# Optimization experiments

Measured on AMD Instinct MI355X. Metric: run time of the kernel, lower is better.

The kernel has to match this reference:

```python
import math
import jax, jax.numpy as jnp
import numpy as np

B, S, DK, DV = 8, 2048, 512, 512

def setup_inputs() -> dict:
    key = jax.random.key(0)
    kq, kk, kv, km = jax.random.split(key, 4)
    Q = jax.random.normal(kq, (B, S, DK), dtype=jnp.float32)
    K = jax.random.normal(kk, (B, S, DK), dtype=jnp.float32)
    V = jax.random.normal(kv, (B, S, DV), dtype=jnp.float32)
    # key-padding mask, True = masked out; broadcasts over query dim
    mask_out = jax.random.randint(km, (B, 1, S), 0, 2).astype(jnp.bool_)
    return {"Q": Q, "K": K, "V": V, "mask_out": mask_out}

def reference(Q, K, V, mask_out):
    scale = math.sqrt(Q.shape[-1])
    # [B, S, S] scores
    scores = jnp.einsum('bqd,bkd->bqk', Q, K) / scale
    scores = jnp.where(mask_out, -jnp.inf, scores)
    attn = jax.nn.softmax(scores, axis=-1)
    # dropout is identity in eval mode (reference baseline)
    return jnp.einsum('bqk,bkv->bqv', attn, V)
```

## Files before the change

kernel.cpp:

```cpp
#include <hip/hip_runtime.h>
#include <stdint.h>
#include <stddef.h>

#define B_ 8
#define S_ 2048
#define D_ 512
#define QT 64
#define KTL 32
#define NIT (S_ / KTL)

typedef __attribute__((ext_vector_type(8))) short short8;
typedef __attribute__((ext_vector_type(4))) float f32x4;

#define OFF_K0  0
#define OFF_K1  32768
#define OFF_ST  65536
#define OFF_P   73728
#define OFF_A   77824
#define OFF_L   78080
#define OFF_M   78336
#define LDS_BYTES 78592

__device__ __forceinline__ void gl_lds16(const void* g, void* l) {
  __builtin_amdgcn_global_load_lds(
      (const __attribute__((address_space(1))) uint32_t*)g,
      (__attribute__((address_space(3))) uint32_t*)l, 16, 0, 0);
}

__device__ __forceinline__ void bar_lgkm() {
  __asm__ __volatile__("" ::: "memory");
  __builtin_amdgcn_s_waitcnt(0xC07F);
  __builtin_amdgcn_s_barrier();
  __asm__ __volatile__("" ::: "memory");
}
__device__ __forceinline__ void bar_vm0() {
  __asm__ __volatile__("" ::: "memory");
  __builtin_amdgcn_s_waitcnt(0x0070);
  __builtin_amdgcn_s_barrier();
  __asm__ __volatile__("" ::: "memory");
}

template<int CTRL>
__device__ __forceinline__ float dpp_mov(float x) {
  return __builtin_bit_cast(float,
      __builtin_amdgcn_update_dpp(0, __builtin_bit_cast(int, x),
                                  CTRL, 0xF, 0xF, true));
}
__device__ __forceinline__ float red8_max(float x) {
  x = fmaxf(x, dpp_mov<0xB1>(x));
  x = fmaxf(x, dpp_mov<0x4E>(x));
  x = fmaxf(x, dpp_mov<0x141>(x));
  return x;
}
__device__ __forceinline__ float red8_sum(float x) {
  x += dpp_mov<0xB1>(x);
  x += dpp_mov<0x4E>(x);
  x += dpp_mov<0x141>(x);
  return x;
}

__device__ __forceinline__ uint32_t f2bf(float f) {
  union { float f; uint32_t u; } x; x.f = f;
  uint32_t r = x.u + 0x7FFFu + ((x.u >> 16) & 1u);
  return r >> 16;
}

__device__ __forceinline__ bool sniff_fp32(const void* p) {
  const uint32_t* w = (const uint32_t*)p;
  bool ok = true;
  #pragma unroll 1
  for (int i = 0; i < 64; ++i) {
    uint32_t e = (w[i] >> 23) & 0xFFu;
    if (!(e == 0u || (e >= 64u && e <= 192u))) ok = false;
  }
  return ok;
}

__device__ __forceinline__ short8 cvt8(const void* src, bool fp32) {
  short8 d;
  if (fp32) {
    const float* s = (const float*)src;
    f32x4 a = *(const f32x4*)s, c = *(const f32x4*)(s + 4);
    #pragma unroll
    for (int j = 0; j < 4; ++j) { d[j] = (short)f2bf(a[j]); d[4 + j] = (short)f2bf(c[j]); }
  } else {
    d = *(const short8*)src;
  }
  return d;
}

__global__ void prep_kernel(const void* __restrict__ K, const void* __restrict__ V,
                            uint16_t* __restrict__ kbf, uint16_t* __restrict__ vt) {
  __shared__ uint32_t vtile[64 * 32];
  bool fp32 = sniff_fp32(K);
  int kt = blockIdx.x, dt = blockIdx.y, b = blockIdx.z;
  int t  = threadIdx.x;
  {
    size_t off = (size_t)b * S_ * D_ + (size_t)(kt * 64 + (t >> 3)) * D_ + dt * 64 + (t & 7) * 8;
    const void* src = fp32 ? (const void*)((const float*)K + off)
                           : (const void*)((const uint16_t*)K + off);
    *(short8*)(kbf + off) = cvt8(src, fp32);
  }
  {
    int key = t >> 3;
    int c0  = (t & 7) * 4;
    size_t off = (size_t)b * S_ * D_ + (size_t)(kt * 64 + key) * D_ + dt * 64 + (t & 7) * 8;
    const void* src = fp32 ? (const void*)((const float*)V + off)
                           : (const void*)((const uint16_t*)V + off);
    short8 d = cvt8(src, fp32);
    const uint32_t* dw = (const uint32_t*)&d;
    #pragma unroll
    for (int i = 0; i < 4; ++i)
      vtile[key * 32 + ((c0 + i + key) & 31)] = dw[i];
  }
  __syncthreads();
  {
    int dvl = t >> 3;
    int kg  = t & 7;
    short8 o;
    #pragma unroll
    for (int j = 0; j < 8; ++j) {
      int key = kg * 8 + j;
      uint32_t wv = vtile[key * 32 + (((dvl >> 1) + key) & 31)];
      o[j] = (short)((dvl & 1) ? (wv >> 16) : (wv & 0xFFFFu));
    }
    *(short8*)(vt + ((size_t)b * D_ + dt * 64 + dvl) * S_ + kt * 64 + kg * 8) = o;
  }
}

__device__ __forceinline__ void stage_K(char* buf, const uint16_t* kg, int w, int lane, int kt) {
  #pragma unroll
  for (int p = 0; p < 4; ++p) {
    int n = p * 8 + w;
    int g = (lane & ~7) | ((lane ^ n) & 7);
    gl_lds16(kg + ((size_t)(kt * KTL + n)) * D_ + g * 8, buf + n * 1024);
  }
}
__device__ __forceinline__ void stage_K_slow(char* buf, const void* kg, bool fp32,
                                             int w, int lane, int kt) {
  #pragma unroll
  for (int p = 0; p < 4; ++p) {
    int n = p * 8 + w;
    size_t off = ((size_t)(kt * KTL + n)) * D_ + lane * 8;
    const void* src = fp32 ? (const void*)((const float*)kg + off)
                           : (const void*)((const uint16_t*)kg + off);
    short8 d = cvt8(src, fp32);
    int s = (lane & ~7) | ((lane ^ n) & 7);
    *(short8*)(buf + n * 1024 + s * 16) = d;
  }
}
__device__ __forceinline__ void stage_V_slow(char* smem, const void* vg, bool fp32,
                                             int w, int lane, int kt) {
  #pragma unroll
  for (int p = 0; p < 4; ++p) {
    int n = p * 8 + w;
    size_t off = ((size_t)(kt * KTL + n)) * D_ + lane * 8;
    const void* src = fp32 ? (const void*)((const float*)vg + off)
                           : (const void*)((const uint16_t*)vg + off);
    short8 d = cvt8(src, fp32);
    *(short8*)(smem + OFF_K1 + n * 1024 + lane * 16) = d;
  }
}

template<bool FAST>
__global__ __launch_bounds__(512, 2)
void attn_kernel(const void* __restrict__ Q, const void* __restrict__ K,
                 const void* __restrict__ V, const void* __restrict__ mask,
                 const uint16_t* __restrict__ kbf, const uint16_t* __restrict__ vtbf,
                 void* __restrict__ out) {
  extern __shared__ char smem[];
  const int tid  = threadIdx.x;
  const int lane = tid & 63;
  const int w    = tid >> 6;
  const int m15  = lane & 15;
  const int kq   = lane >> 4;

  const bool fp32 = sniff_fp32(Q);

  const int b     = blockIdx.x;
  const int qbase = blockIdx.y * QT;
  const int qt_w  = w >> 1;
  const int kh    = w & 1;

  const uint16_t* kgf  = FAST ? (kbf + (size_t)b * S_ * D_) : nullptr;
  const uint16_t* vtg  = FAST ? (vtbf + (size_t)b * D_ * S_) : nullptr;
  const void* kgs = fp32 ? (const void*)((const float*)K + (size_t)b * S_ * D_)
                         : (const void*)((const uint16_t*)K + (size_t)b * S_ * D_);
  const void* vgs = fp32 ? (const void*)((const float*)V + (size_t)b * S_ * D_)
                         : (const void*)((const uint16_t*)V + (size_t)b * S_ * D_);

  if (tid < 64) {
    const uint32_t* mw = (const uint32_t*)mask;
    const uint8_t*  mb = (const uint8_t*)mask;
    bool is64 = true, any_even = false, is32 = true;
    for (int j = 0; j < 64; ++j) {
      uint32_t lo = mw[2 * j], hi = mw[2 * j + 1];
      if (hi != 0u || lo > 1u) is64 = false;
      if (lo) any_even = true;
    }
    is64 = is64 && any_even;
    for (int j = 0; j < 128; ++j) {
      uint32_t x = mw[j];
      if (x != 0u && x != 1u && x != 0x3F800000u) is32 = false;
    }
    uint32_t bits = 0;
    int base = b * S_ + tid * 32;
    for (int e = 0; e < 32; ++e) {
      uint32_t x = is64 ? mw[2 * (base + e)]
                        : (is32 ? mw[base + e] : (uint32_t)mb[base + e]);
      bits |= (x ? 1u : 0u) << e;
    }
    *(uint32_t*)(smem + OFF_M + tid * 4) = bits;
  }

  short8 aq[16];
  {
    size_t q0 = ((size_t)b * S_ + qbase + qt_w * 16 + m15) * D_ + kq * 8;
    #pragma unroll
    for (int sl = 0; sl < 16; ++sl) {
      size_t off = q0 + sl * 32;
      const void* src = fp32 ? (const void*)((const float*)Q + off)
                             : (const void*)((const uint16_t*)Q + off);
      aq[sl] = cvt8(src, fp32);
    }
  }

  f32x4 acc_o[4][4];
  #pragma unroll
  for (int i = 0; i < 4; ++i)
    #pragma unroll
    for (int j = 0; j < 4; ++j)
      acc_o[i][j] = (f32x4){0.f, 0.f, 0.f, 0.f};

  float m_run = -1e30f, l_run = 0.f;
  const float k1 = 0.06375872f;

  if (FAST) stage_K(smem + OFF_K0, kgf, w, lane, 0);

  for (int kt = 0; kt < NIT; ++kt) {
    char* kbuf = smem + ((kt & 1) && FAST ? OFF_K1 : OFF_K0);
    if (FAST) {
      bar_vm0();
    } else {
      __syncthreads();
      stage_K_slow(smem + OFF_K0, kgs, fp32, w, lane, kt);
      stage_V_slow(smem, vgs, fp32, w, lane, kt);
      __syncthreads();
    }

    short8 vf[4];
    if (FAST) {
      #pragma unroll
      for (int ct = 0; ct < 4; ++ct)
        vf[ct] = *(const short8*)(vtg + (size_t)(w * 64 + ct * 16 + m15) * S_
                                  + kt * KTL + kq * 8);
      if (kt < NIT - 1)
        stage_K(smem + ((kt & 1) ? OFF_K0 : OFF_K1), kgf, w, lane, kt + 1);
    }

    int keyg = kt * KTL + kh * 16 + m15;
    float bv = ((*(const uint32_t*)(smem + OFF_M + (keyg >> 5) * 4) >> (keyg & 31)) & 1u)
               ? -3.0e38f : 0.f;

    const int n = kh * 16 + m15;
    f32x4 acc_s0 = (f32x4){0.f, 0.f, 0.f, 0.f};
    f32x4 acc_s1 = (f32x4){0.f, 0.f, 0.f, 0.f};
    #pragma unroll
    for (int sl = 0; sl < 8; ++sl) {
      int c0  = sl * 4 + kq;
      int c1  = (sl + 8) * 4 + kq;
      int cs0 = (c0 & ~7) | ((c0 ^ n) & 7);
      int cs1 = (c1 & ~7) | ((c1 ^ n) & 7);
      short8 bf0 = *(const short8*)(kbuf + n * 1024 + cs0 * 16);
      short8 bf1 = *(const short8*)(kbuf + n * 1024 + cs1 * 16);
      acc_s0 = __builtin_amdgcn_mfma_f32_16x16x32_bf16(aq[sl],     bf0, acc_s0, 0, 0, 0);
      acc_s1 = __builtin_amdgcn_mfma_f32_16x16x32_bf16(aq[sl + 8], bf1, acc_s1, 0, 0, 0);
    }

    {
      int key  = n;
      int blk  = qt_w * 4 + kq;
      int xblk = blk ^ (key & 15) ^ ((key >> 2) & 3);
      f32x4 sv;
      #pragma unroll
      for (int r = 0; r < 4; ++r) sv[r] = (acc_s0[r] + acc_s1[r]) * k1 + bv;
      *(f32x4*)(smem + OFF_ST + key * 256 + xblk * 16) = sv;
    }
    bar_lgkm();

    {
      int r  = w * 8 + (lane >> 3);
      int k0 = (lane & 7) * 4;
      float u[4];
      #pragma unroll
      for (int i = 0; i < 4; ++i) {
        int k    = k0 + i;
        int xblk = (r >> 2) ^ (k & 15) ^ ((k >> 2) & 3);
        u[i] = *(const float*)(smem + OFF_ST + k * 256 + xblk * 16 + (r & 3) * 4);
      }
      float mt = fmaxf(fmaxf(u[0], u[1]), fmaxf(u[2], u[3]));
      mt = red8_max(mt);
      float m_new = fmaxf(m_run, mt);
      float alpha = exp2f(m_run - m_new);
      float s = 0.f;
      #pragma unroll
      for (int i = 0; i < 4; ++i) { u[i] = exp2f(u[i] - m_new); s += u[i]; }
      s = red8_sum(s);
      l_run = l_run * alpha + s;
      m_run = m_new;
      uint2 d;
      d.x = f2bf(u[0]) | (f2bf(u[1]) << 16);
      d.y = f2bf(u[2]) | (f2bf(u[3]) << 16);
      int g = ((lane & 7) >> 1) ^ (r & 3);
      *(uint2*)(smem + OFF_P + r * 64 + g * 16 + (lane & 1) * 8) = d;
      if ((lane & 7) == 0) {
        *(float*)(smem + OFF_A + r * 4) = alpha;
        *(float*)(smem + OFF_L + r * 4) = l_run;
      }
    }
    bar_lgkm();

    #pragma unroll
    for (int rt = 0; rt < 4; ++rt) {
      f32x4 al = *(const f32x4*)(smem + OFF_A + (rt * 16 + kq * 4) * 4);
      #pragma unroll
      for (int ct = 0; ct < 4; ++ct) acc_o[rt][ct] *= al;
    }
    short8 ap[4];
    #pragma unroll
    for (int rt = 0; rt < 4; ++rt) {
      int rr = rt * 16 + m15;
      int g  = kq ^ (rr & 3);
      ap[rt] = *(const short8*)(smem + OFF_P + rr * 64 + g * 16);
    }
    #pragma unroll
    for (int ct = 0; ct < 4; ++ct) {
      short8 bvv;
      if (FAST) {
        bvv = vf[ct];
      } else {
        #pragma unroll
        for (int j = 0; j < 8; ++j)
          bvv[j] = *(const short*)(smem + OFF_K1 + (kq * 8 + j) * 1024
                                   + (w * 64 + ct * 16 + m15) * 2);
      }
      #pragma unroll
      for (int rt = 0; rt < 4; ++rt)
        acc_o[rt][ct] = __builtin_amdgcn_mfma_f32_16x16x32_bf16(
            ap[rt], bvv, acc_o[rt][ct], 0, 0, 0);
    }
  }

  #pragma unroll
  for (int rt = 0; rt < 4; ++rt) {
    f32x4 lv = *(const f32x4*)(smem + OFF_L + (rt * 16 + kq * 4) * 4);
    f32x4 inv;
    #pragma unroll
    for (int r = 0; r < 4; ++r) inv[r] = lv[r] > 0.f ? 1.f / lv[r] : 0.f;
    #pragma unroll
    for (int ct = 0; ct < 4; ++ct) {
      int col = w * 64 + ct * 16 + m15;
      #pragma unroll
      for (int r = 0; r < 4; ++r) {
        int row = qbase + rt * 16 + kq * 4 + r;
        size_t idx = ((size_t)b * S_ + row) * D_ + col;
        float val = acc_o[rt][ct][r] * inv[r];
        if (fp32) ((float*)out)[idx] = val;
        else      ((uint16_t*)out)[idx] = (uint16_t)f2bf(val);
      }
    }
  }
}

extern "C" void kernel_launch(void* const* d_in, const int* in_sizes, int n_in,
                              void* d_out, int out_size, void* d_ws, size_t ws_size,
                              hipStream_t stream) {
  (void)in_sizes; (void)n_in; (void)out_size;
  const void* Q    = d_in[0];
  const void* K    = d_in[1];
  const void* V    = d_in[2];
  const void* mask = d_in[3];

  const size_t half = (size_t)B_ * S_ * D_ * 2;
  bool fast = ws_size >= 2 * half;

  if (fast) {
    uint16_t* kbf  = (uint16_t*)d_ws;
    uint16_t* vtbf = (uint16_t*)((char*)d_ws + half);
    prep_kernel<<<dim3(32, 8, 8), 512, 0, stream>>>(K, V, kbf, vtbf);
    hipFuncSetAttribute((const void*)attn_kernel<true>,
                        hipFuncAttributeMaxDynamicSharedMemorySize, LDS_BYTES);
    attn_kernel<true><<<dim3(8, S_ / QT), 512, LDS_BYTES, stream>>>(
        Q, K, V, mask, kbf, vtbf, d_out);
  } else {
    hipFuncSetAttribute((const void*)attn_kernel<false>,
                        hipFuncAttributeMaxDynamicSharedMemorySize, LDS_BYTES);
    attn_kernel<false><<<dim3(8, S_ / QT), 512, LDS_BYTES, stream>>>(
        Q, K, V, mask, nullptr, nullptr, d_out);
  }
}
```

Measured before the change: 293.1 us.

## Load K fragments directly from global memory instead of double-buffered LDS staging

Removes the async global-to-LDS double-buffered staging of K tiles in the fast path. Each lane now reads its K operand fragments straight from global memory (relying on L2/L1 caching) before the MFMA loop, and the per-iteration vmcnt barrier is dropped. This saves LDS traffic and a barrier, but the QK MFMAs now wait on global-load latency without prefetch overlap, and the same K rows are read redundantly by multiple waves.

```diff
diff --git a/kernel.cpp b/kernel.cpp
--- a/kernel.cpp
+++ b/kernel.cpp
@@ -21,21 +21,9 @@
 #define OFF_M   78336
 #define LDS_BYTES 78592
 
-__device__ __forceinline__ void gl_lds16(const void* g, void* l) {
-  __builtin_amdgcn_global_load_lds(
-      (const __attribute__((address_space(1))) uint32_t*)g,
-      (__attribute__((address_space(3))) uint32_t*)l, 16, 0, 0);
-}
-
 __device__ __forceinline__ void bar_lgkm() {
   __asm__ __volatile__("" ::: "memory");
   __builtin_amdgcn_s_waitcnt(0xC07F);
-  __builtin_amdgcn_s_barrier();
-  __asm__ __volatile__("" ::: "memory");
-}
-__device__ __forceinline__ void bar_vm0() {
-  __asm__ __volatile__("" ::: "memory");
-  __builtin_amdgcn_s_waitcnt(0x0070);
   __builtin_amdgcn_s_barrier();
   __asm__ __volatile__("" ::: "memory");
 }
@@ -128,14 +116,6 @@
   }
 }
 
-__device__ __forceinline__ void stage_K(char* buf, const uint16_t* kg, int w, int lane, int kt) {
-  #pragma unroll
-  for (int p = 0; p < 4; ++p) {
-    int n = p * 8 + w;
-    int g = (lane & ~7) | ((lane ^ n) & 7);
-    gl_lds16(kg + ((size_t)(kt * KTL + n)) * D_ + g * 8, buf + n * 1024);
-  }
-}
 __device__ __forceinline__ void stage_K_slow(char* buf, const void* kg, bool fp32,
                                              int w, int lane, int kt) {
   #pragma unroll
@@ -235,12 +215,18 @@
   float m_run = -1e30f, l_run = 0.f;
   const float k1 = 0.06375872f;
 
-  if (FAST) stage_K(smem + OFF_K0, kgf, w, lane, 0);
-
+  const int nql = kh * 16 + m15;
+
+  if (FAST) __syncthreads();
+
+  #pragma unroll 1
   for (int kt = 0; kt < NIT; ++kt) {
-    char* kbuf = smem + ((kt & 1) && FAST ? OFF_K1 : OFF_K0);
+    short8 vf[4];
     if (FAST) {
-      bar_vm0();
+      #pragma unroll
+      for (int ct = 0; ct < 4; ++ct)
+        vf[ct] = *(const short8*)(vtg + (size_t)(w * 64 + ct * 16 + m15) * S_
+                                  + kt * KTL + kq * 8);
     } else {
       __syncthreads();
       stage_K_slow(smem + OFF_K0, kgs, fp32, w, lane, kt);
@@ -248,43 +234,41 @@
       __syncthreads();
     }
 
-    short8 vf[4];
-    if (FAST) {
-      #pragma unroll
-      for (int ct = 0; ct < 4; ++ct)
-        vf[ct] = *(const short8*)(vtg + (size_t)(w * 64 + ct * 16 + m15) * S_
-                                  + kt * KTL + kq * 8);
-      if (kt < NIT - 1)
-        stage_K(smem + ((kt & 1) ? OFF_K0 : OFF_K1), kgf, w, lane, kt + 1);
-    }
-
-    int keyg = kt * KTL + kh * 16 + m15;
-    float bv = ((*(const uint32_t*)(smem + OFF_M + (keyg >> 5) * 4) >> (keyg & 31)) & 1u)
-               ? -3.0e38f : 0.f;
-
-    const int n = kh * 16 + m15;
     f32x4 acc_s0 = (f32x4){0.f, 0.f, 0.f, 0.f};
     f32x4 acc_s1 = (f32x4){0.f, 0.f, 0.f, 0.f};
-    #pragma unroll
-    for (int sl = 0; sl < 8; ++sl) {
-      int c0  = sl * 4 + kq;
-      int c1  = (sl + 8) * 4 + kq;
-      int cs0 = (c0 & ~7) | ((c0 ^ n) & 7);
-      int cs1 = (c1 & ~7) | ((c1 ^ n) & 7);
-      short8 bf0 = *(const short8*)(kbuf + n * 1024 + cs0 * 16);
-      short8 bf1 = *(const short8*)(kbuf + n * 1024 + cs1 * 16);
-      acc_s0 = __builtin_amdgcn_mfma_f32_16x16x32_bf16(aq[sl],     bf0, acc_s0, 0, 0, 0);
-      acc_s1 = __builtin_amdgcn_mfma_f32_16x16x32_bf16(aq[sl + 8], bf1, acc_s1, 0, 0, 0);
+    if (FAST) {
+      const uint16_t* kp = kgf + ((size_t)(kt * KTL + nql)) * D_ + kq * 8;
+      #pragma unroll
+      for (int sl = 0; sl < 8; ++sl) {
+        short8 b0 = *(const short8*)(kp + sl * 32);
+        short8 b1 = *(const short8*)(kp + (sl + 8) * 32);
+        acc_s0 = __builtin_amdgcn_mfma_f32_16x16x32_bf16(aq[sl],     b0, acc_s0, 0, 0, 0);
+        acc_s1 = __builtin_amdgcn_mfma_f32_16x16x32_bf16(aq[sl + 8], b1, acc_s1, 0, 0, 0);
+      }
+    } else {
+      #pragma unroll
+      for (int sl = 0; sl < 8; ++sl) {
+        int c0  = sl * 4 + kq;
+        int c1  = (sl + 8) * 4 + kq;
+        int cs0 = (c0 & ~7) | ((c0 ^ nql) & 7);
+        int cs1 = (c1 & ~7) | ((c1 ^ nql) & 7);
+        short8 b0 = *(const short8*)(smem + OFF_K0 + nql * 1024 + cs0 * 16);
+        short8 b1 = *(const short8*)(smem + OFF_K0 + nql * 1024 + cs1 * 16);
+        acc_s0 = __builtin_amdgcn_mfma_f32_16x16x32_bf16(aq[sl],     b0, acc_s0, 0, 0, 0);
+        acc_s1 = __builtin_amdgcn_mfma_f32_16x16x32_bf16(aq[sl + 8], b1, acc_s1, 0, 0, 0);
+      }
     }
 
     {
-      int key  = n;
+      int keyg = kt * KTL + nql;
+      float bv = ((*(const uint32_t*)(smem + OFF_M + (keyg >> 5) * 4) >> (keyg & 31)) & 1u)
+                 ? -3.0e38f : 0.f;
       int blk  = qt_w * 4 + kq;
-      int xblk = blk ^ (key & 15) ^ ((key >> 2) & 3);
+      int xblk = blk ^ (nql & 15) ^ ((nql >> 2) & 3);
       f32x4 sv;
       #pragma unroll
       for (int r = 0; r < 4; ++r) sv[r] = (acc_s0[r] + acc_s1[r]) * k1 + bv;
-      *(f32x4*)(smem + OFF_ST + key * 256 + xblk * 16) = sv;
+      *(f32x4*)(smem + OFF_ST + nql * 256 + xblk * 16) = sv;
     }
     bar_lgkm();
 
```

After: 446.7 us. 52.4% more time.

## Compute softmax in registers via transposed MFMA, dropping score staging through LDS

Applied to the files above, without the earlier changes.

In the fast path the QK^T MFMA operands are swapped so that each lane holds scores for a single query row. The online softmax can then run in registers, using cross-lane shuffles plus a small LDS exchange of half-tile maxima. This removes the score-tile store and reload through LDS and one of the per-iteration reductions. The mask is read as one 32-bit word per tile, and l is summed from the two halves at the end. The slow path is split into its own constexpr branch and left unchanged. The cost is an extra small LDS region and slightly more complex index bookkeeping.

```diff
diff --git a/kernel.cpp b/kernel.cpp
--- a/kernel.cpp
+++ b/kernel.cpp
@@ -17,9 +17,10 @@
 #define OFF_ST  65536
 #define OFF_P   73728
 #define OFF_A   77824
-#define OFF_L   78080
-#define OFF_M   78336
-#define LDS_BYTES 78592
+#define OFF_HM  78080
+#define OFF_L   78592
+#define OFF_M   79104
+#define LDS_BYTES 79360
 
 __device__ __forceinline__ void gl_lds16(const void* g, void* l) {
   __builtin_amdgcn_global_load_lds(
@@ -235,138 +236,225 @@
   float m_run = -1e30f, l_run = 0.f;
   const float k1 = 0.06375872f;
 
-  if (FAST) stage_K(smem + OFF_K0, kgf, w, lane, 0);
-
-  for (int kt = 0; kt < NIT; ++kt) {
-    char* kbuf = smem + ((kt & 1) && FAST ? OFF_K1 : OFF_K0);
-    if (FAST) {
+  const int nql = kh * 16 + m15;
+  const int qsw = qt_w * 16 + m15;
+
+  if constexpr (FAST) {
+    stage_K(smem + OFF_K0, kgf, w, lane, 0);
+
+    #pragma unroll 1
+    for (int kt = 0; kt < NIT; ++kt) {
+      char* kbuf = smem + ((kt & 1) ? OFF_K1 : OFF_K0);
       bar_vm0();
-    } else {
-      __syncthreads();
-      stage_K_slow(smem + OFF_K0, kgs, fp32, w, lane, kt);
-      stage_V_slow(smem, vgs, fp32, w, lane, kt);
-      __syncthreads();
-    }
-
-    short8 vf[4];
-    if (FAST) {
+
+      short8 vf[4];
       #pragma unroll
       for (int ct = 0; ct < 4; ++ct)
         vf[ct] = *(const short8*)(vtg + (size_t)(w * 64 + ct * 16 + m15) * S_
                                   + kt * KTL + kq * 8);
       if (kt < NIT - 1)
         stage_K(smem + ((kt & 1) ? OFF_K0 : OFF_K1), kgf, w, lane, kt + 1);
-    }
-
-    int keyg = kt * KTL + kh * 16 + m15;
-    float bv = ((*(const uint32_t*)(smem + OFF_M + (keyg >> 5) * 4) >> (keyg & 31)) & 1u)
-               ? -3.0e38f : 0.f;
-
-    const int n = kh * 16 + m15;
-    f32x4 acc_s0 = (f32x4){0.f, 0.f, 0.f, 0.f};
-    f32x4 acc_s1 = (f32x4){0.f, 0.f, 0.f, 0.f};
-    #pragma unroll
-    for (int sl = 0; sl < 8; ++sl) {
-      int c0  = sl * 4 + kq;
-      int c1  = (sl + 8) * 4 + kq;
-      int cs0 = (c0 & ~7) | ((c0 ^ n) & 7);
-      int cs1 = (c1 & ~7) | ((c1 ^ n) & 7);
-      short8 bf0 = *(const short8*)(kbuf + n * 1024 + cs0 * 16);
-      short8 bf1 = *(const short8*)(kbuf + n * 1024 + cs1 * 16);
-      acc_s0 = __builtin_amdgcn_mfma_f32_16x16x32_bf16(aq[sl],     bf0, acc_s0, 0, 0, 0);
-      acc_s1 = __builtin_amdgcn_mfma_f32_16x16x32_bf16(aq[sl + 8], bf1, acc_s1, 0, 0, 0);
-    }
-
-    {
-      int key  = n;
-      int blk  = qt_w * 4 + kq;
-      int xblk = blk ^ (key & 15) ^ ((key >> 2) & 3);
-      f32x4 sv;
-      #pragma unroll
-      for (int r = 0; r < 4; ++r) sv[r] = (acc_s0[r] + acc_s1[r]) * k1 + bv;
-      *(f32x4*)(smem + OFF_ST + key * 256 + xblk * 16) = sv;
-    }
-    bar_lgkm();
-
-    {
-      int r  = w * 8 + (lane >> 3);
-      int k0 = (lane & 7) * 4;
+
+      f32x4 acc_s0 = (f32x4){0.f, 0.f, 0.f, 0.f};
+      f32x4 acc_s1 = (f32x4){0.f, 0.f, 0.f, 0.f};
+      #pragma unroll
+      for (int sl = 0; sl < 8; ++sl) {
+        int c0  = sl * 4 + kq;
+        int c1  = (sl + 8) * 4 + kq;
+        int cs0 = (c0 & ~7) | ((c0 ^ nql) & 7);
+        int cs1 = (c1 & ~7) | ((c1 ^ nql) & 7);
+        short8 b0 = *(const short8*)(kbuf + nql * 1024 + cs0 * 16);
+        short8 b1 = *(const short8*)(kbuf + nql * 1024 + cs1 * 16);
+        acc_s0 = __builtin_amdgcn_mfma_f32_16x16x32_bf16(b0, aq[sl],     acc_s0, 0, 0, 0);
+        acc_s1 = __builtin_amdgcn_mfma_f32_16x16x32_bf16(b1, aq[sl + 8], acc_s1, 0, 0, 0);
+      }
+
+      uint32_t mword = *(const uint32_t*)(smem + OFF_M + kt * 4);
       float u[4];
       #pragma unroll
-      for (int i = 0; i < 4; ++i) {
-        int k    = k0 + i;
-        int xblk = (r >> 2) ^ (k & 15) ^ ((k >> 2) & 3);
-        u[i] = *(const float*)(smem + OFF_ST + k * 256 + xblk * 16 + (r & 3) * 4);
-      }
-      float mt = fmaxf(fmaxf(u[0], u[1]), fmaxf(u[2], u[3]));
-      mt = red8_max(mt);
-      float m_new = fmaxf(m_run, mt);
+      for (int r = 0; r < 4; ++r) {
+        float bv = ((mword >> (kh * 16 + kq * 4 + r)) & 1u) ? -3.0e38f : 0.f;
+        u[r] = (acc_s0[r] + acc_s1[r]) * k1 + bv;
+      }
+      float hm = fmaxf(fmaxf(u[0], u[1]), fmaxf(u[2], u[3]));
+      hm = fmaxf(hm, __shfl_xor(hm, 16, 64));
+      hm = fmaxf(hm, __shfl_xor(hm, 32, 64));
+      if (lane < 16)
+        *(float*)(smem + OFF_HM + qsw * 8 + kh * 4) = hm;
+      bar_lgkm();
+
+      float other = *(const float*)(smem + OFF_HM + qsw * 8 + (1 - kh) * 4);
+      float m_new = fmaxf(m_run, fmaxf(hm, other));
       float alpha = exp2f(m_run - m_new);
+      m_run = m_new;
       float s = 0.f;
       #pragma unroll
-      for (int i = 0; i < 4; ++i) { u[i] = exp2f(u[i] - m_new); s += u[i]; }
-      s = red8_sum(s);
+      for (int r = 0; r < 4; ++r) { u[r] = exp2f(u[r] - m_new); s += u[r]; }
+      s += __shfl_xor(s, 16, 64);
+      s += __shfl_xor(s, 32, 64);
       l_run = l_run * alpha + s;
-      m_run = m_new;
       uint2 d;
       d.x = f2bf(u[0]) | (f2bf(u[1]) << 16);
       d.y = f2bf(u[2]) | (f2bf(u[3]) << 16);
-      int g = ((lane & 7) >> 1) ^ (r & 3);
-      *(uint2*)(smem + OFF_P + r * 64 + g * 16 + (lane & 1) * 8) = d;
-      if ((lane & 7) == 0) {
-        *(float*)(smem + OFF_A + r * 4) = alpha;
-        *(float*)(smem + OFF_L + r * 4) = l_run;
-      }
-    }
-    bar_lgkm();
+      int g0 = kh * 2 + (kq >> 1);
+      int g  = g0 ^ (qsw & 3);
+      *(uint2*)(smem + OFF_P + qsw * 64 + g * 16 + (kq & 1) * 8) = d;
+      if (kh == 0 && lane < 16)
+        *(float*)(smem + OFF_A + qsw * 4) = alpha;
+      bar_lgkm();
+
+      #pragma unroll
+      for (int rt = 0; rt < 4; ++rt) {
+        f32x4 al = *(const f32x4*)(smem + OFF_A + (rt * 16 + kq * 4) * 4);
+        #pragma unroll
+        for (int ct = 0; ct < 4; ++ct) acc_o[rt][ct] *= al;
+      }
+      short8 ap[4];
+      #pragma unroll
+      for (int rt = 0; rt < 4; ++rt) {
+        int rr = rt * 16 + m15;
+        int gg = kq ^ (rr & 3);
+        ap[rt] = *(const short8*)(smem + OFF_P + rr * 64 + gg * 16);
+      }
+      #pragma unroll
+      for (int ct = 0; ct < 4; ++ct)
+        #pragma unroll
+        for (int rt = 0; rt < 4; ++rt)
+          acc_o[rt][ct] = __builtin_amdgcn_mfma_f32_16x16x32_bf16(
+              ap[rt], vf[ct], acc_o[rt][ct], 0, 0, 0);
+    }
+
+    if (lane < 16)
+      *(float*)(smem + OFF_L + qsw * 8 + kh * 4) = l_run;
+    __syncthreads();
 
     #pragma unroll
     for (int rt = 0; rt < 4; ++rt) {
-      f32x4 al = *(const f32x4*)(smem + OFF_A + (rt * 16 + kq * 4) * 4);
-      #pragma unroll
-      for (int ct = 0; ct < 4; ++ct) acc_o[rt][ct] *= al;
-    }
-    short8 ap[4];
-    #pragma unroll
-    for (int rt = 0; rt < 4; ++rt) {
-      int rr = rt * 16 + m15;
-      int g  = kq ^ (rr & 3);
-      ap[rt] = *(const short8*)(smem + OFF_P + rr * 64 + g * 16);
-    }
-    #pragma unroll
-    for (int ct = 0; ct < 4; ++ct) {
-      short8 bvv;
-      if (FAST) {
-        bvv = vf[ct];
-      } else {
+      #pragma unroll
+      for (int ct = 0; ct < 4; ++ct) {
+        int col = w * 64 + ct * 16 + m15;
+        #pragma unroll
+        for (int r = 0; r < 4; ++r) {
+          int row = rt * 16 + kq * 4 + r;
+          float lt = *(const float*)(smem + OFF_L + row * 8)
+                   + *(const float*)(smem + OFF_L + row * 8 + 4);
+          float inv = lt > 0.f ? 1.f / lt : 0.f;
+          size_t idx = ((size_t)b * S_ + qbase + row) * D_ + col;
+          float val = acc_o[rt][ct][r] * inv;
+          if (fp32) ((float*)out)[idx] = val;
+          else      ((uint16_t*)out)[idx] = (uint16_t)f2bf(val);
+        }
+      }
+    }
+  } else {
+    #pragma unroll 1
+    for (int kt = 0; kt < NIT; ++kt) {
+      __syncthreads();
+      stage_K_slow(smem + OFF_K0, kgs, fp32, w, lane, kt);
+      stage_V_slow(smem, vgs, fp32, w, lane, kt);
+      __syncthreads();
+
+      int keyg = kt * KTL + nql;
+      float bv = ((*(const uint32_t*)(smem + OFF_M + (keyg >> 5) * 4) >> (keyg & 31)) & 1u)
+                 ? -3.0e38f : 0.f;
+      f32x4 a0 = {0.f,0.f,0.f,0.f}, a1 = {0.f,0.f,0.f,0.f};
+      #pragma unroll
+      for (int sl = 0; sl < 8; ++sl) {
+        int c0  = sl * 4 + kq;
+        int c1  = (sl + 8) * 4 + kq;
+        int cs0 = (c0 & ~7) | ((c0 ^ nql) & 7);
+        int cs1 = (c1 & ~7) | ((c1 ^ nql) & 7);
+        short8 bf0 = *(const short8*)(smem + OFF_K0 + nql * 1024 + cs0 * 16);
+        short8 bf1 = *(const short8*)(smem + OFF_K0 + nql * 1024 + cs1 * 16);
+        a0 = __builtin_amdgcn_mfma_f32_16x16x32_bf16(aq[sl],     bf0, a0, 0, 0, 0);
+        a1 = __builtin_amdgcn_mfma_f32_16x16x32_bf16(aq[sl + 8], bf1, a1, 0, 0, 0);
+      }
+      {
+        int blk  = qt_w * 4 + kq;
+        int xblk = blk ^ (nql & 15) ^ ((nql >> 2) & 3);
+        f32x4 sv;
+        #pragma unroll
+        for (int r = 0; r < 4; ++r) sv[r] = (a0[r] + a1[r]) * k1 + bv;
+        *(f32x4*)(smem + OFF_ST + nql * 256 + xblk * 16) = sv;
+      }
+      bar_lgkm();
+
+      {
+        int r  = w * 8 + (lane >> 3);
+        int k0 = (lane & 7) * 4;
+        float u[4];
+        #pragma unroll
+        for (int i = 0; i < 4; ++i) {
+          int k    = k0 + i;
+          int xblk = (r >> 2) ^ (k & 15) ^ ((k >> 2) & 3);
+          u[i] = *(const float*)(smem + OFF_ST + k * 256 + xblk * 16 + (r & 3) * 4);
+        }
+        float mt = fmaxf(fmaxf(u[0], u[1]), fmaxf(u[2], u[3]));
+        mt = red8_max(mt);
+        float m_new = fmaxf(m_run, mt);
+        float alpha = exp2f(m_run - m_new);
+        float s = 0.f;
+        #pragma unroll
+        for (int i = 0; i < 4; ++i) { u[i] = exp2f(u[i] - m_new); s += u[i]; }
+        s = red8_sum(s);
+        l_run = l_run * alpha + s;
+        m_run = m_new;
+        uint2 d;
+        d.x = f2bf(u[0]) | (f2bf(u[1]) << 16);
+        d.y = f2bf(u[2]) | (f2bf(u[3]) << 16);
+        int g = ((lane & 7) >> 1) ^ (r & 3);
+        *(uint2*)(smem + OFF_P + r * 64 + g * 16 + (lane & 1) * 8) = d;
+        if ((lane & 7) == 0) {
+          *(float*)(smem + OFF_A + r * 4) = alpha;
+          *(float*)(smem + OFF_L + r * 4) = l_run;
+        }
+      }
+      bar_lgkm();
+
+      #pragma unroll
+      for (int rt = 0; rt < 4; ++rt) {
+        f32x4 al = *(const f32x4*)(smem + OFF_A + (rt * 16 + kq * 4) * 4);
+        #pragma unroll
+        for (int ct = 0; ct < 4; ++ct) acc_o[rt][ct] *= al;
+      }
+      short8 ap[4];
+      #pragma unroll
+      for (int rt = 0; rt < 4; ++rt) {
+        int rr = rt * 16 + m15;
+        int g  = kq ^ (rr & 3);
+        ap[rt] = *(const short8*)(smem + OFF_P + rr * 64 + g * 16);
+      }
+      #pragma unroll
+      for (int ct = 0; ct < 4; ++ct) {
+        short8 bvv;
         #pragma unroll
         for (int j = 0; j < 8; ++j)
           bvv[j] = *(const short*)(smem + OFF_K1 + (kq * 8 + j) * 1024
                                    + (w * 64 + ct * 16 + m15) * 2);
-      }
-      #pragma unroll
-      for (int rt = 0; rt < 4; ++rt)
-        acc_o[rt][ct] = __builtin_amdgcn_mfma_f32_16x16x32_bf16(
-            ap[rt], bvv, acc_o[rt][ct], 0, 0, 0);
-    }
-  }
-
-  #pragma unroll
-  for (int rt = 0; rt < 4; ++rt) {
-    f32x4 lv = *(const f32x4*)(smem + OFF_L + (rt * 16 + kq * 4) * 4);
-    f32x4 inv;
-    #pragma unroll
-    for (int r = 0; r < 4; ++r) inv[r] = lv[r] > 0.f ? 1.f / lv[r] : 0.f;
-    #pragma unroll
-    for (int ct = 0; ct < 4; ++ct) {
-      int col = w * 64 + ct * 16 + m15;
-      #pragma unroll
-      for (int r = 0; r < 4; ++r) {
-        int row = qbase + rt * 16 + kq * 4 + r;
-        size_t idx = ((size_t)b * S_ + row) * D_ + col;
-        float val = acc_o[rt][ct][r] * inv[r];
-        if (fp32) ((float*)out)[idx] = val;
-        else      ((uint16_t*)out)[idx] = (uint16_t)f2bf(val);
+        #pragma unroll
+        for (int rt = 0; rt < 4; ++rt)
+          acc_o[rt][ct] = __builtin_amdgcn_mfma_f32_16x16x32_bf16(
+              ap[rt], bvv, acc_o[rt][ct], 0, 0, 0);
+      }
+    }
+
+    #pragma unroll
+    for (int rt = 0; rt < 4; ++rt) {
+      f32x4 lv = *(const f32x4*)(smem + OFF_L + (rt * 16 + kq * 4) * 4);
+      f32x4 inv;
+      #pragma unroll
+      for (int r = 0; r < 4; ++r) inv[r] = lv[r] > 0.f ? 1.f / lv[r] : 0.f;
+      #pragma unroll
+      for (int ct = 0; ct < 4; ++ct) {
+        int col = w * 64 + ct * 16 + m15;
+        #pragma unroll
+        for (int r = 0; r < 4; ++r) {
+          int row = qbase + rt * 16 + kq * 4 + r;
+          size_t idx = ((size_t)b * S_ + row) * D_ + col;
+          float val = acc_o[rt][ct][r] * inv[r];
+          if (fp32) ((float*)out)[idx] = val;
+          else      ((uint16_t*)out)[idx] = (uint16_t)f2bf(val);
+        }
       }
     }
   }
```

After: 306.9 us. 4.7% more time.
